# Kernel optimization log

Measured on AMD Instinct MI355X. Metric: run time of the kernel, lower is better.

The kernel has to match this reference:

```python
import jax, jax.numpy as jnp
import numpy as np

B, S, HIDDEN = 8, 2048, 1024
NUM_GROUPS, NUM_VARS = 2, 320
CODEVECTOR_DIM = 256
TAU = 2.0  # module hardcodes self.temperature = 2
EPS_U = 1e-6


def setup_inputs() -> dict:
    key = jax.random.key(0)
    k1, k2, k3, k4 = jax.random.split(key, 4)
    hidden_states = jax.random.normal(k1, (B, S, HIDDEN), dtype=jnp.float32)
    W = jax.random.normal(k2, (NUM_GROUPS * NUM_VARS, HIDDEN), dtype=jnp.float32) * 0.02
    b = jnp.zeros((NUM_GROUPS * NUM_VARS,), dtype=jnp.float32)
    codevectors = jax.random.normal(
        k3, (1, NUM_GROUPS * NUM_VARS, CODEVECTOR_DIM // NUM_GROUPS), dtype=jnp.float32)
    gumbel_u = jax.random.uniform(
        k4, (B * S * NUM_GROUPS, NUM_VARS), minval=EPS_U, maxval=1.0 - EPS_U, dtype=jnp.float32)
    return {"hidden_states": hidden_states, "W": W, "b": b,
            "codevectors": codevectors, "gumbel_u": gumbel_u}


def reference(hidden_states, W, b, codevectors, gumbel_u):
    Bs, Ss, H = hidden_states.shape
    G, V = NUM_GROUPS, NUM_VARS
    N = Bs * Ss
    # weight_proj: [B,S,H] -> [B,S,G*V]
    logits = jnp.einsum('bsh,vh->bsv', hidden_states, W) + b
    logits = logits.reshape(N * G, V)
    # gumbel_softmax(tau=2, hard=True) -- training path
    gumbel = -jnp.log(-jnp.log(gumbel_u))
    y_soft = jax.nn.softmax((logits + gumbel) / TAU, axis=-1)
    idx = jnp.argmax(y_soft, axis=-1)
    y_hard = jax.nn.one_hot(idx, V, dtype=y_soft.dtype)
    # straight-through (hard value, soft gradient)
    codevector_probs = y_hard + y_soft - jax.lax.stop_gradient(y_soft)
    # perplexity over the soft (non-gumbel) distribution
    soft_dist = jax.nn.softmax(logits.reshape(N, G, V), axis=-1)
    marginal = soft_dist.mean(axis=0)                      # [G, V]
    perplexity = jnp.exp(-jnp.sum(marginal * jnp.log(marginal + 1e-7), axis=-1)).sum()
    # one-hot probs x codevectors, grouped sum: [N,G,V] x [G,V,d] -> [N,G,d]
    cv = codevectors.reshape(G, V, CODEVECTOR_DIM // G)
    out = jnp.einsum('ngv,gvd->ngd', codevector_probs.reshape(N, G, V), cv)
    out = out.reshape(Bs, Ss, CODEVECTOR_DIM)
    return out, perplexity
```

## Files before the change

### kernel.cpp

```cpp
#include <hip/hip_runtime.h>
#include <math.h>

#define NROWS 16384
#define HIDDEN 1024
#define NVARS 320
#define NCOLS 640
#define CVDIM 256
#define OUT_ELEMS (NROWS * CVDIM)
#define NSHADOW 32

typedef __attribute__((ext_vector_type(8))) short short8;
typedef __attribute__((ext_vector_type(4))) float floatx4;

__device__ __forceinline__ unsigned f32_to_bf16(float f) {
    unsigned u = __builtin_bit_cast(unsigned, f);
    return (u + 0x7FFFu + ((u >> 16) & 1u)) >> 16;
}
__device__ __forceinline__ float bf16_to_f32(ushort u) {
    return __builtin_bit_cast(float, ((unsigned)u) << 16);
}

__global__ __launch_bounds__(256) void convert_bf16_kernel(
    const float* __restrict__ src, ushort* __restrict__ dst, int n8)
{
    const int i = blockIdx.x * 256 + threadIdx.x;
    if (i >= n8) return;
    const float4* s = reinterpret_cast<const float4*>(src) + (size_t)i * 2;
    const float4 v0 = s[0];
    const float4 v1 = s[1];
    uint4 p;
    p.x = f32_to_bf16(v0.x) | (f32_to_bf16(v0.y) << 16);
    p.y = f32_to_bf16(v0.z) | (f32_to_bf16(v0.w) << 16);
    p.z = f32_to_bf16(v1.x) | (f32_to_bf16(v1.y) << 16);
    p.w = f32_to_bf16(v1.z) | (f32_to_bf16(v1.w) << 16);
    reinterpret_cast<uint4*>(dst)[i] = p;
}

__device__ __forceinline__ void async16(const void* g, void* l) {
    __builtin_amdgcn_global_load_lds(
        (const __attribute__((address_space(1))) void*)g,
        (__attribute__((address_space(3))) void*)l,
        16, 0, 0);
}

#define GBM 128
#define GBN 128
#define GBK 32

__global__ __launch_bounds__(256) void gemm_logits_kernel(
    const ushort* __restrict__ Xbf,
    const ushort* __restrict__ Wbf,
    const float* __restrict__ bias,
    ushort* __restrict__ Lg)
{
    __shared__ __align__(16) ushort As[4096];
    __shared__ __align__(16) ushort Bs[4096];

    const int tid = threadIdx.x;
    const int lane = tid & 63;
    const int w = tid >> 6;
    const int wm = w >> 1, wn = w & 1;

    const int m0 = blockIdx.x * GBM;
    const int n0 = blockIdx.y * GBN;

    const int rm = lane & 15;
    const int kc = lane >> 4;

    floatx4 acc[4][4];
#pragma unroll
    for (int i = 0; i < 4; ++i)
#pragma unroll
        for (int j = 0; j < 4; ++j) acc[i][j] = (floatx4){0.f, 0.f, 0.f, 0.f};

    const int rowc0 = tid >> 2, sub0 = (tid & 3) * 8;
    const int rowc1 = (tid + 256) >> 2;

    for (int k0 = 0; k0 < HIDDEN; k0 += GBK) {
        async16(Xbf + (size_t)(m0 + rowc0) * HIDDEN + k0 + sub0, As + tid * 8);
        async16(Xbf + (size_t)(m0 + rowc1) * HIDDEN + k0 + sub0, As + (tid + 256) * 8);
        async16(Wbf + (size_t)(n0 + rowc0) * HIDDEN + k0 + sub0, Bs + tid * 8);
        async16(Wbf + (size_t)(n0 + rowc1) * HIDDEN + k0 + sub0, Bs + (tid + 256) * 8);
        __syncthreads();

        const short8* Asv = reinterpret_cast<const short8*>(As);
        const short8* Bsv = reinterpret_cast<const short8*>(Bs);
        short8 af[4], bfr[4];
#pragma unroll
        for (int f = 0; f < 4; ++f) {
            af[f]  = Asv[(wm * 64 + f * 16 + rm) * 4 + kc];
            bfr[f] = Bsv[(wn * 64 + f * 16 + rm) * 4 + kc];
        }
#pragma unroll
        for (int i = 0; i < 4; ++i)
#pragma unroll
            for (int j = 0; j < 4; ++j)
                acc[i][j] = __builtin_amdgcn_mfma_f32_16x16x32_bf16(
                    af[i], bfr[j], acc[i][j], 0, 0, 0);
        __syncthreads();
    }

    const int cl = lane & 15;
    const int r4 = (lane >> 4) * 4;
    float bj[4];
#pragma unroll
    for (int j = 0; j < 4; ++j) bj[j] = bias[n0 + wn * 64 + j * 16 + cl];

#pragma unroll
    for (int i = 0; i < 4; ++i)
#pragma unroll
        for (int j = 0; j < 4; ++j) {
            const int col = n0 + wn * 64 + j * 16 + cl;
#pragma unroll
            for (int q = 0; q < 4; ++q) {
                const int row = m0 + wm * 64 + i * 16 + r4 + q;
                unsigned v = f32_to_bf16(acc[i][j][q] + bj[j]);
                unsigned o = (unsigned)__shfl_xor((int)v, 1);
                if ((cl & 1) == 0)
                    *reinterpret_cast<uint*>(Lg + (size_t)row * NCOLS + col) =
                        v | (o << 16);
            }
        }
}

__global__ __launch_bounds__(256) void quantize_kernel(
    const ushort* __restrict__ Lg,
    const float* __restrict__ gu,
    const float* __restrict__ cv,
    float* __restrict__ out,
    float* __restrict__ shadow)
{
    __shared__ float smr[4][NCOLS];
    const int tid = threadIdx.x;
    const int w = tid >> 6;
    const int lane = tid & 63;

    const int n = blockIdx.x * 4 + w;

    float lg[2][5], ug[2][5];
    const ushort* lp = Lg + (size_t)n * NCOLS + lane;
    const float* gp = gu + (size_t)(2 * n) * NVARS + lane;
#pragma unroll
    for (int g = 0; g < 2; ++g)
#pragma unroll
        for (int j = 0; j < 5; ++j) {
            lg[g][j] = bf16_to_f32(lp[g * NVARS + j * 64]);
            ug[g][j] = gp[g * NVARS + j * 64];
        }

    int bi[2];
#pragma unroll
    for (int g = 0; g < 2; ++g) {
        float bk = lg[g][0] - __logf(-__logf(ug[g][0]));
        int b = lane;
#pragma unroll
        for (int j = 1; j < 5; ++j) {
            const float kj = lg[g][j] - __logf(-__logf(ug[g][j]));
            const int v = lane + j * 64;
            if (kj > bk) { bk = kj; b = v; }
        }
#pragma unroll
        for (int sh = 32; sh > 0; sh >>= 1) {
            const float ok = __shfl_xor(bk, sh);
            const int oi = __shfl_xor(b, sh);
            if (ok > bk || (ok == bk && oi < b)) { bk = ok; b = oi; }
        }
        bi[g] = b;
    }

    const float2 c0 = reinterpret_cast<const float2*>(cv + (size_t)bi[0] * 128)[lane];
    const float2 c1 = reinterpret_cast<const float2*>(cv + (size_t)(NVARS + bi[1]) * 128)[lane];

#pragma unroll
    for (int g = 0; g < 2; ++g) {
        float p[5], sume = 0.f;
#pragma unroll
        for (int j = 0; j < 5; ++j) { p[j] = __expf(lg[g][j]); sume += p[j]; }
#pragma unroll
        for (int sh = 32; sh > 0; sh >>= 1) sume += __shfl_xor(sume, sh);
        const float inv = 1.f / sume;
#pragma unroll
        for (int j = 0; j < 5; ++j)
            smr[w][g * NVARS + lane + j * 64] = p[j] * inv;
    }

    float2* orow = reinterpret_cast<float2*>(out + (size_t)n * CVDIM);
    orow[lane] = c0;
    orow[64 + lane] = c1;

    __syncthreads();
    float* sh0 = shadow + (blockIdx.x & (NSHADOW - 1)) * NCOLS;
    for (int i = tid; i < NCOLS; i += 256)
        atomicAdd(&sh0[i], smr[0][i] + smr[1][i] + smr[2][i] + smr[3][i]);
}

__global__ void perplexity_kernel(const float* __restrict__ shadow,
                                  float* __restrict__ out)
{
    const int lane = threadIdx.x;
    float h0 = 0.0f, h1 = 0.0f;
    for (int v = lane; v < NVARS; v += 64) {
        float s0 = 0.f, s1 = 0.f;
#pragma unroll
        for (int sh = 0; sh < NSHADOW; ++sh) {
            s0 += shadow[sh * NCOLS + v];
            s1 += shadow[sh * NCOLS + NVARS + v];
        }
        const float m0 = s0 * (1.0f / (float)NROWS);
        h0 += m0 * logf(m0 + 1e-7f);
        const float m1 = s1 * (1.0f / (float)NROWS);
        h1 += m1 * logf(m1 + 1e-7f);
    }
#pragma unroll
    for (int s = 32; s > 0; s >>= 1) {
        h0 += __shfl_xor(h0, s);
        h1 += __shfl_xor(h1, s);
    }
    if (lane == 0) out[OUT_ELEMS] = expf(-h0) + expf(-h1);
}

extern "C" void kernel_launch(void* const* d_in, const int* in_sizes, int n_in,
                              void* d_out, int out_size, void* d_ws, size_t ws_size,
                              hipStream_t stream) {
    const float* X    = (const float*)d_in[0];
    const float* W    = (const float*)d_in[1];
    const float* bias = (const float*)d_in[2];
    const float* cv   = (const float*)d_in[3];
    const float* gu   = (const float*)d_in[4];
    float* out = (float*)d_out;

    ushort* Xbf    = (ushort*)d_ws;
    ushort* Wbf    = Xbf + (size_t)NROWS * HIDDEN;
    ushort* Lg     = Wbf + (size_t)NCOLS * HIDDEN;
    float*  shadow = (float*)(Lg + (size_t)NROWS * NCOLS);

    (void)hipMemsetAsync(shadow, 0, NSHADOW * NCOLS * sizeof(float), stream);

    convert_bf16_kernel<<<NROWS * HIDDEN / 8 / 256, 256, 0, stream>>>(
        X, Xbf, NROWS * HIDDEN / 8);
    convert_bf16_kernel<<<(NCOLS * HIDDEN / 8 + 255) / 256, 256, 0, stream>>>(
        W, Wbf, NCOLS * HIDDEN / 8);

    dim3 ggrid(NROWS / GBM, NCOLS / GBN);
    gemm_logits_kernel<<<ggrid, 256, 0, stream>>>(Xbf, Wbf, bias, Lg);

    quantize_kernel<<<NROWS / 4, 256, 0, stream>>>(Lg, gu, cv, out, shadow);

    perplexity_kernel<<<1, 64, 0, stream>>>(shadow, out);
}
```

Before: 82.25 us.

## Fold shadow memset into convert kernel, halve quantize blocks, widen perplexity

The separate memset of the shadow accumulation buffer is removed and its zeroing is folded into the X conversion kernel, saving one stream operation. The quantize kernel now handles two rows per wavefront (n and n+8192), which halves the grid and the number of shadow atomics per row. The perplexity reduction uses 256 threads instead of 64. These cut launch count and atomic traffic in exchange for more registers per quantize thread.

```diff
diff --git a/kernel.cpp b/kernel.cpp
--- a/kernel.cpp
+++ b/kernel.cpp
@@ -21,9 +21,11 @@
 }
 
 __global__ __launch_bounds__(256) void convert_bf16_kernel(
-    const float* __restrict__ src, ushort* __restrict__ dst, int n8)
+    const float* __restrict__ src, ushort* __restrict__ dst, int n8,
+    float* __restrict__ zbuf, int zn)
 {
     const int i = blockIdx.x * 256 + threadIdx.x;
+    if (i < zn) zbuf[i] = 0.0f;
     if (i >= n8) return;
     const float4* s = reinterpret_cast<const float4*>(src) + (size_t)i * 2;
     const float4 v0 = s[0];
@@ -135,58 +137,78 @@
     const int w = tid >> 6;
     const int lane = tid & 63;
 
-    const int n = blockIdx.x * 4 + w;
-
-    float lg[2][5], ug[2][5];
-    const ushort* lp = Lg + (size_t)n * NCOLS + lane;
-    const float* gp = gu + (size_t)(2 * n) * NVARS + lane;
-#pragma unroll
-    for (int g = 0; g < 2; ++g)
-#pragma unroll
-        for (int j = 0; j < 5; ++j) {
-            lg[g][j] = bf16_to_f32(lp[g * NVARS + j * 64]);
-            ug[g][j] = gp[g * NVARS + j * 64];
-        }
-
-    int bi[2];
+    const int n0 = blockIdx.x * 4 + w;
+    const int n1 = n0 + 8192;
+
+    float lg[2][2][5], ug[2][2][5];
+#pragma unroll
+    for (int r = 0; r < 2; ++r) {
+        const int n = r ? n1 : n0;
+        const ushort* lp = Lg + (size_t)n * NCOLS + lane;
+        const float* gp = gu + (size_t)(2 * n) * NVARS + lane;
+#pragma unroll
+        for (int g = 0; g < 2; ++g)
+#pragma unroll
+            for (int j = 0; j < 5; ++j) {
+                lg[r][g][j] = bf16_to_f32(lp[g * NVARS + j * 64]);
+                ug[r][g][j] = gp[g * NVARS + j * 64];
+            }
+    }
+
+    int bi[2][2];
+#pragma unroll
+    for (int r = 0; r < 2; ++r)
+#pragma unroll
+        for (int g = 0; g < 2; ++g) {
+            float bk = lg[r][g][0] - __logf(-__logf(ug[r][g][0]));
+            int b = lane;
+#pragma unroll
+            for (int j = 1; j < 5; ++j) {
+                const float kj = lg[r][g][j] - __logf(-__logf(ug[r][g][j]));
+                const int v = lane + j * 64;
+                if (kj > bk) { bk = kj; b = v; }
+            }
+#pragma unroll
+            for (int sh = 32; sh > 0; sh >>= 1) {
+                const float ok = __shfl_xor(bk, sh);
+                const int oi = __shfl_xor(b, sh);
+                if (ok > bk || (ok == bk && oi < b)) { bk = ok; b = oi; }
+            }
+            bi[r][g] = b;
+        }
+
+    float2 c[2][2];
+#pragma unroll
+    for (int r = 0; r < 2; ++r) {
+        c[r][0] = reinterpret_cast<const float2*>(cv + (size_t)bi[r][0] * 128)[lane];
+        c[r][1] = reinterpret_cast<const float2*>(cv + (size_t)(NVARS + bi[r][1]) * 128)[lane];
+    }
+
 #pragma unroll
     for (int g = 0; g < 2; ++g) {
-        float bk = lg[g][0] - __logf(-__logf(ug[g][0]));
-        int b = lane;
-#pragma unroll
-        for (int j = 1; j < 5; ++j) {
-            const float kj = lg[g][j] - __logf(-__logf(ug[g][j]));
-            const int v = lane + j * 64;
-            if (kj > bk) { bk = kj; b = v; }
-        }
-#pragma unroll
-        for (int sh = 32; sh > 0; sh >>= 1) {
-            const float ok = __shfl_xor(bk, sh);
-            const int oi = __shfl_xor(b, sh);
-            if (ok > bk || (ok == bk && oi < b)) { bk = ok; b = oi; }
-        }
-        bi[g] = b;
-    }
-
-    const float2 c0 = reinterpret_cast<const float2*>(cv + (size_t)bi[0] * 128)[lane];
-    const float2 c1 = reinterpret_cast<const float2*>(cv + (size_t)(NVARS + bi[1]) * 128)[lane];
-
-#pragma unroll
-    for (int g = 0; g < 2; ++g) {
-        float p[5], sume = 0.f;
-#pragma unroll
-        for (int j = 0; j < 5; ++j) { p[j] = __expf(lg[g][j]); sume += p[j]; }
-#pragma unroll
-        for (int sh = 32; sh > 0; sh >>= 1) sume += __shfl_xor(sume, sh);
-        const float inv = 1.f / sume;
+        float pr[2][5];
+#pragma unroll
+        for (int r = 0; r < 2; ++r) {
+            float sume = 0.f;
+#pragma unroll
+            for (int j = 0; j < 5; ++j) { pr[r][j] = __expf(lg[r][g][j]); sume += pr[r][j]; }
+#pragma unroll
+            for (int sh = 32; sh > 0; sh >>= 1) sume += __shfl_xor(sume, sh);
+            const float inv = 1.f / sume;
+#pragma unroll
+            for (int j = 0; j < 5; ++j) pr[r][j] *= inv;
+        }
 #pragma unroll
         for (int j = 0; j < 5; ++j)
-            smr[w][g * NVARS + lane + j * 64] = p[j] * inv;
-    }
-
-    float2* orow = reinterpret_cast<float2*>(out + (size_t)n * CVDIM);
-    orow[lane] = c0;
-    orow[64 + lane] = c1;
+            smr[w][g * NVARS + lane + j * 64] = pr[0][j] + pr[1][j];
+    }
+
+    float2* o0 = reinterpret_cast<float2*>(out + (size_t)n0 * CVDIM);
+    o0[lane] = c[0][0];
+    o0[64 + lane] = c[0][1];
+    float2* o1 = reinterpret_cast<float2*>(out + (size_t)n1 * CVDIM);
+    o1[lane] = c[1][0];
+    o1[64 + lane] = c[1][1];
 
     __syncthreads();
     float* sh0 = shadow + (blockIdx.x & (NSHADOW - 1)) * NCOLS;
@@ -194,29 +216,30 @@
         atomicAdd(&sh0[i], smr[0][i] + smr[1][i] + smr[2][i] + smr[3][i]);
 }
 
-__global__ void perplexity_kernel(const float* __restrict__ shadow,
-                                  float* __restrict__ out)
-{
-    const int lane = threadIdx.x;
-    float h0 = 0.0f, h1 = 0.0f;
-    for (int v = lane; v < NVARS; v += 64) {
-        float s0 = 0.f, s1 = 0.f;
-#pragma unroll
-        for (int sh = 0; sh < NSHADOW; ++sh) {
-            s0 += shadow[sh * NCOLS + v];
-            s1 += shadow[sh * NCOLS + NVARS + v];
-        }
-        const float m0 = s0 * (1.0f / (float)NROWS);
-        h0 += m0 * logf(m0 + 1e-7f);
-        const float m1 = s1 * (1.0f / (float)NROWS);
-        h1 += m1 * logf(m1 + 1e-7f);
+__global__ __launch_bounds__(256) void perplexity_kernel(
+    const float* __restrict__ shadow, float* __restrict__ out)
+{
+    __shared__ float r0[4], r1[4];
+    const int tid = threadIdx.x;
+    float h0 = 0.f, h1 = 0.f;
+    for (int cidx = tid; cidx < NCOLS; cidx += 256) {
+        float s = 0.f;
+#pragma unroll
+        for (int sh = 0; sh < NSHADOW; ++sh) s += shadow[sh * NCOLS + cidx];
+        const float m = s * (1.0f / (float)NROWS);
+        const float t = m * logf(m + 1e-7f);
+        if (cidx < NVARS) h0 += t; else h1 += t;
     }
 #pragma unroll
     for (int s = 32; s > 0; s >>= 1) {
         h0 += __shfl_xor(h0, s);
         h1 += __shfl_xor(h1, s);
     }
-    if (lane == 0) out[OUT_ELEMS] = expf(-h0) + expf(-h1);
+    if ((tid & 63) == 0) { r0[tid >> 6] = h0; r1[tid >> 6] = h1; }
+    __syncthreads();
+    if (tid == 0)
+        out[OUT_ELEMS] = expf(-(r0[0] + r0[1] + r0[2] + r0[3])) +
+                         expf(-(r1[0] + r1[1] + r1[2] + r1[3]));
 }
 
 extern "C" void kernel_launch(void* const* d_in, const int* in_sizes, int n_in,
@@ -234,17 +257,15 @@
     ushort* Lg     = Wbf + (size_t)NCOLS * HIDDEN;
     float*  shadow = (float*)(Lg + (size_t)NROWS * NCOLS);
 
-    (void)hipMemsetAsync(shadow, 0, NSHADOW * NCOLS * sizeof(float), stream);
-
     convert_bf16_kernel<<<NROWS * HIDDEN / 8 / 256, 256, 0, stream>>>(
-        X, Xbf, NROWS * HIDDEN / 8);
+        X, Xbf, NROWS * HIDDEN / 8, shadow, NSHADOW * NCOLS);
     convert_bf16_kernel<<<(NCOLS * HIDDEN / 8 + 255) / 256, 256, 0, stream>>>(
-        W, Wbf, NCOLS * HIDDEN / 8);
+        W, Wbf, NCOLS * HIDDEN / 8, (float*)nullptr, 0);
 
     dim3 ggrid(NROWS / GBM, NCOLS / GBN);
     gemm_logits_kernel<<<ggrid, 256, 0, stream>>>(Xbf, Wbf, bias, Lg);
 
-    quantize_kernel<<<NROWS / 4, 256, 0, stream>>>(Lg, gu, cv, out, shadow);
-
-    perplexity_kernel<<<1, 64, 0, stream>>>(shadow, out);
-}
+    quantize_kernel<<<NROWS / 2 / 4, 256, 0, stream>>>(Lg, gu, cv, out, shadow);
+
+    perplexity_kernel<<<1, 256, 0, stream>>>(shadow, out);
+}
```

Measured after the change: 75.08 us. 1.1x faster.
